# Kernel optimization log

Measured on AMD Instinct MI355X. Metric: run time of the kernel, lower is better.

Reference implementation:

```python
import jax, jax.numpy as jnp
import numpy as np

# graph layout constants
B = 64        # number of graphs
NPG = 512     # nodes per graph
N = B * NPG   # total nodes
DEG = 16      # avg degree
E = N * DEG   # total edges
F_IN = 256
H, C = 4, 64  # heads, per-head dim
K = NPG // 2  # topk pooling keeps ratio=0.5 per graph


def setup_inputs() -> dict:
    key = jax.random.key(0)
    ks = jax.random.split(key, 8)
    x = jax.random.normal(ks[0], (N, F_IN), dtype=jnp.float32)
    # within-graph random edges (src -> dst), contiguous node ids per graph
    offs = jnp.repeat(jnp.arange(B, dtype=jnp.int64) * NPG, NPG * DEG)
    src = offs + jax.random.randint(ks[1], (E,), 0, NPG)
    dst = offs + jax.random.randint(ks[2], (E,), 0, NPG)
    edge_index = jnp.stack([src, dst]).astype(jnp.int64)
    W = jax.random.normal(ks[3], (F_IN, H, C), dtype=jnp.float32) / np.sqrt(F_IN)
    att_src = jax.random.normal(ks[4], (H, C), dtype=jnp.float32) / np.sqrt(C)
    att_dst = jax.random.normal(ks[5], (H, C), dtype=jnp.float32) / np.sqrt(C)
    bias = jnp.zeros((H * C,), dtype=jnp.float32)
    bn_gamma = jnp.ones((H * C,), dtype=jnp.float32)
    bn_beta = jnp.zeros((H * C,), dtype=jnp.float32)
    pool_weight = jax.random.normal(ks[6], (H * C,), dtype=jnp.float32) / np.sqrt(H * C)
    return {"x": x, "edge_index": edge_index, "W": W, "att_src": att_src,
            "att_dst": att_dst, "bias": bias, "bn_gamma": bn_gamma,
            "bn_beta": bn_beta, "pool_weight": pool_weight}


def reference(x, edge_index, W, att_src, att_dst, bias, bn_gamma, bn_beta, pool_weight):
    n = x.shape[0]
    # --- GATConv ---
    h = jnp.einsum('nf,fhc->nhc', x, W)                 # [N,H,C]
    a_src = jnp.sum(h * att_src, axis=-1)               # [N,H]
    a_dst = jnp.sum(h * att_dst, axis=-1)               # [N,H]
    loops = jnp.arange(n, dtype=edge_index.dtype)        # add_self_loops=True default
    src = jnp.concatenate([edge_index[0], loops])
    dst = jnp.concatenate([edge_index[1], loops])
    e = jax.nn.leaky_relu(a_src[src] + a_dst[dst], 0.2)  # [E+N,H]
    # scatter-softmax over edges grouped by destination node
    emax = jax.ops.segment_max(e, dst, num_segments=n)
    ex = jnp.exp(e - emax[dst])
    den = jax.ops.segment_sum(ex, dst, num_segments=n)
    alpha = ex / (den[dst] + 1e-16)                      # [E+N,H]
    msg = alpha[:, :, None] * h[src]                     # [E+N,H,C]
    out = jax.ops.segment_sum(msg, dst, num_segments=n)  # [N,H,C]
    feat = out.reshape(n, H * C) + bias                  # concat heads
    # --- ReLU + BatchNorm (batch stats, training mode) ---
    feat = jax.nn.relu(feat)
    mean = jnp.mean(feat, axis=0)
    var = jnp.var(feat, axis=0)
    feat = (feat - mean) * jax.lax.rsqrt(var + 1e-5) * bn_gamma + bn_beta
    # --- TopKPooling (score = x.w/||w||, keep top ratio per graph, gate by tanh) ---
    score = feat @ pool_weight / jnp.linalg.norm(pool_weight)  # [N]
    top_s, top_i = jax.lax.top_k(score.reshape(B, NPG), K)     # [B,K]
    fg = feat.reshape(B, NPG, H * C)
    sel = jnp.take_along_axis(fg, top_i[:, :, None], axis=1)    # [B,K,HC]
    pooled = sel * jnp.tanh(top_s)[:, :, None]
    return pooled.reshape(B * K, H * C)
```

## Files before the change

### kernel.cpp

```cpp
#include <hip/hip_runtime.h>
#include <math.h>

#define N_NODES 32768
#define NPG 512
#define NGRAPH 64
#define KKEEP 256
#define CAP 64

typedef __attribute__((ext_vector_type(8))) short short8;
typedef __attribute__((ext_vector_type(4))) float f32x4;

__device__ __forceinline__ unsigned short f2bf(float v) {
  unsigned u = __builtin_bit_cast(unsigned, v);
  u = (u + 0x7FFFu + ((u >> 16) & 1u)) >> 16;
  return (unsigned short)u;
}
__device__ __forceinline__ float bf2f(unsigned short u) {
  unsigned v = ((unsigned)u) << 16;
  return __builtin_bit_cast(float, v);
}

__device__ __forceinline__ void async_cp16(unsigned short* l, const unsigned short* g) {
  __builtin_amdgcn_global_load_lds(
      (const __attribute__((address_space(1))) unsigned int*)g,
      (__attribute__((address_space(3))) unsigned int*)l, 16, 0, 0);
}

__device__ __forceinline__ void block_barrier() {
  __builtin_amdgcn_sched_barrier(0);
  asm volatile("s_barrier" ::: "memory");
  __builtin_amdgcn_sched_barrier(0);
}
__device__ __forceinline__ void wait_all() {
  asm volatile("s_waitcnt vmcnt(0) lgkmcnt(0)" ::: "memory");
  __builtin_amdgcn_sched_barrier(0);
}

__global__ __launch_bounds__(256) void k_conv(
    const float* __restrict__ W,
    unsigned short* __restrict__ wth, unsigned short* __restrict__ wtl,
    unsigned short* __restrict__ wtll, int* __restrict__ cnt) {
  const int t = threadIdx.x;
  if (blockIdx.x >= 64) {
    int i = (blockIdx.x - 64) * 1024 + t * 4;
    *(int4*)&cnt[i] = make_int4(0, 0, 0, 0);
    return;
  }
  int n = blockIdx.x * 4 + (t >> 6);
  int k = (t & 63) * 4;
  unsigned short hb[4], lb[4], qb[4];
#pragma unroll
  for (int j = 0; j < 4; j++) {
    float v = W[(size_t)(k + j) * 256 + n];
    unsigned short hh = f2bf(v);
    float e1 = v - bf2f(hh);
    unsigned short ll = f2bf(e1);
    float e2 = e1 - bf2f(ll);
    hb[j] = hh; lb[j] = ll; qb[j] = f2bf(e2);
  }
  *(uint2*)&wth[(size_t)n * 256 + k] = *(uint2*)&hb[0];
  *(uint2*)&wtl[(size_t)n * 256 + k] = *(uint2*)&lb[0];
  *(uint2*)&wtll[(size_t)n * 256 + k] = *(uint2*)&qb[0];
}

#define A_STR 129
#define B_BASE 12384
#define B_SZ 12288
__global__ __launch_bounds__(512, 4) void k_gemm_hist(
    const float* __restrict__ x,
    const unsigned short* __restrict__ wth, const unsigned short* __restrict__ wtl,
    const unsigned short* __restrict__ wtll,
    const float* __restrict__ attS, const float* __restrict__ attD,
    float* __restrict__ h, float* __restrict__ a_src, float* __restrict__ a_dst,
    const int* __restrict__ ei, int E, int* __restrict__ cnt,
    unsigned short* __restrict__ nbr) {
  __shared__ unsigned short lds[36960];
  const int t = threadIdx.x;
  const int bid = blockIdx.x;
  if (bid % 3 != 0) {
    int ord = bid - bid / 3 - 1;
    int e = ord * 512 + t;
    if (e < E) {
      int s = ei[e];
      int d = ei[E + e];
      int slot = atomicAdd(&cnt[d], 1);
      if (slot < CAP) nbr[(size_t)d * CAP + slot] = (unsigned short)(s & (NPG - 1));
    }
    return;
  }
  const int g = bid / 3;
  const int p = (3 * g) & 7;
  const int mb = p * 32 + (g >> 4);
  const int nh = (g >> 3) & 1;
  const int row0 = mb * 128;
  const int wid = t >> 6, lane = t & 63;
  const int q = lane >> 4, ln = lane & 15;
  const int wm = (wid >> 1) * 32, wn = (wid & 1) * 64;
  const int sr = t >> 2, scq = t & 3;
  f32x4 acc[2][4] = {};

  {
    size_t ga = (size_t)(row0 + sr) * 256 + scq * 8;
    float4 f0 = *(const float4*)&x[ga];
    float4 f1 = *(const float4*)&x[ga + 4];
    float ff[8] = {f0.x, f0.y, f0.z, f0.w, f1.x, f1.y, f1.z, f1.w};
    unsigned short hs[8], ls[8], qs[8];
#pragma unroll
    for (int j = 0; j < 8; j++) {
      unsigned short hh = f2bf(ff[j]);
      float e1 = ff[j] - bf2f(hh);
      unsigned short ll = f2bf(e1);
      float e2 = e1 - bf2f(ll);
      hs[j] = hh; ls[j] = ll; qs[j] = f2bf(e2);
    }
    *(uint4*)&lds[((0 * 4 + scq) * A_STR + sr) * 8] = *(uint4*)&hs[0];
    *(uint4*)&lds[((1 * 4 + scq) * A_STR + sr) * 8] = *(uint4*)&ls[0];
    *(uint4*)&lds[((2 * 4 + scq) * A_STR + sr) * 8] = *(uint4*)&qs[0];
    size_t gb = (size_t)(nh * 128 + (t & 127)) * 256 + (t >> 7) * 8;
    async_cp16(&lds[B_BASE + 0 * 4096 + t * 8], &wth[gb]);
    async_cp16(&lds[B_BASE + 1 * 4096 + t * 8], &wtl[gb]);
    async_cp16(&lds[B_BASE + 2 * 4096 + t * 8], &wtll[gb]);
  }
  wait_all();
  block_barrier();

  for (int kc = 0; kc < 8; kc++) {
    const int cur = kc & 1;
    float4 f0, f1;
    if (kc < 7) {
      const int k1 = (kc + 1) * 32;
      size_t ga = (size_t)(row0 + sr) * 256 + k1 + scq * 8;
      f0 = *(const float4*)&x[ga];
      f1 = *(const float4*)&x[ga + 4];
      unsigned short* bb = &lds[B_BASE + (cur ^ 1) * B_SZ];
      size_t gb = (size_t)(nh * 128 + (t & 127)) * 256 + k1 + (t >> 7) * 8;
      async_cp16(&bb[0 * 4096 + t * 8], &wth[gb]);
      async_cp16(&bb[1 * 4096 + t * 8], &wtl[gb]);
      async_cp16(&bb[2 * 4096 + t * 8], &wtll[gb]);
    }
    const unsigned short* bc = &lds[B_BASE + cur * B_SZ];
    short8 ah[2], al[2], aq[2];
#pragma unroll
    for (int mt = 0; mt < 2; mt++) {
      int r = wm + mt * 16 + ln;
      ah[mt] = *(const short8*)&lds[((0 * 4 + q) * A_STR + r) * 8];
      al[mt] = *(const short8*)&lds[((1 * 4 + q) * A_STR + r) * 8];
      aq[mt] = *(const short8*)&lds[((2 * 4 + q) * A_STR + r) * 8];
    }
#pragma unroll
    for (int nt = 0; nt < 4; nt++) {
      int r = wn + nt * 16 + ln;
      short8 bh = *(const short8*)&bc[0 * 4096 + (q * 128 + r) * 8];
      short8 bl = *(const short8*)&bc[1 * 4096 + (q * 128 + r) * 8];
      short8 bq = *(const short8*)&bc[2 * 4096 + (q * 128 + r) * 8];
#pragma unroll
      for (int mt = 0; mt < 2; mt++) {
        acc[mt][nt] = __builtin_amdgcn_mfma_f32_16x16x32_bf16(ah[mt], bh, acc[mt][nt], 0, 0, 0);
        acc[mt][nt] = __builtin_amdgcn_mfma_f32_16x16x32_bf16(ah[mt], bl, acc[mt][nt], 0, 0, 0);
        acc[mt][nt] = __builtin_amdgcn_mfma_f32_16x16x32_bf16(al[mt], bh, acc[mt][nt], 0, 0, 0);
        acc[mt][nt] = __builtin_amdgcn_mfma_f32_16x16x32_bf16(ah[mt], bq, acc[mt][nt], 0, 0, 0);
        acc[mt][nt] = __builtin_amdgcn_mfma_f32_16x16x32_bf16(al[mt], bl, acc[mt][nt], 0, 0, 0);
        acc[mt][nt] = __builtin_amdgcn_mfma_f32_16x16x32_bf16(aq[mt], bh, acc[mt][nt], 0, 0, 0);
      }
    }
    unsigned short hs[8], ls[8], qs[8];
    if (kc < 7) {
      float ff[8] = {f0.x, f0.y, f0.z, f0.w, f1.x, f1.y, f1.z, f1.w};
#pragma unroll
      for (int j = 0; j < 8; j++) {
        unsigned short hh = f2bf(ff[j]);
        float e1 = ff[j] - bf2f(hh);
        unsigned short ll = f2bf(e1);
        float e2 = e1 - bf2f(ll);
        hs[j] = hh; ls[j] = ll; qs[j] = f2bf(e2);
      }
    }
    block_barrier();
    if (kc < 7) {
      *(uint4*)&lds[((0 * 4 + scq) * A_STR + sr) * 8] = *(uint4*)&hs[0];
      *(uint4*)&lds[((1 * 4 + scq) * A_STR + sr) * 8] = *(uint4*)&ls[0];
      *(uint4*)&lds[((2 * 4 + scq) * A_STR + sr) * 8] = *(uint4*)&qs[0];
    }
    wait_all();
    block_barrier();
  }

  const int head = nh * 2 + (wid & 1);
  float sA[4], sD[4];
#pragma unroll
  for (int nt = 0; nt < 4; nt++) {
    int n = nh * 128 + wn + nt * 16 + ln;
    sA[nt] = attS[n];
    sD[nt] = attD[n];
  }
  float2* epi = (float2*)lds;
#pragma unroll
  for (int mt = 0; mt < 2; mt++) {
#pragma unroll
    for (int reg = 0; reg < 4; reg++) {
      int m = row0 + wm + mt * 16 + q * 4 + reg;
      float ps = 0.f, pd = 0.f;
#pragma unroll
      for (int nt = 0; nt < 4; nt++) {
        float v = acc[mt][nt][reg];
        h[(size_t)m * 256 + nh * 128 + wn + nt * 16 + ln] = v;
        ps = fmaf(v, sA[nt], ps);
        pd = fmaf(v, sD[nt], pd);
      }
      epi[(((wid * 4 + q) * 8) + mt * 4 + reg) * 18 + (ln ^ (q * 4))] =
          make_float2(ps, pd);
    }
  }
  __syncthreads();
  if (lane < 32) {
    const int rr2 = lane & 7;
    const int q2 = lane >> 3;
    const int base = (((wid * 4 + q2) * 8) + rr2) * 18;
    float ps = 0.f, pd = 0.f;
#pragma unroll
    for (int i = 0; i < 16; i++) {
      float2 v = epi[base + (i ^ (q2 * 4))];
      ps += v.x;
      pd += v.y;
    }
    int m = row0 + wm + (rr2 >> 2) * 16 + q2 * 4 + (rr2 & 3);
    a_src[m * 4 + head] = ps;
    a_dst[m * 4 + head] = pd;
  }
}

__global__ __launch_bounds__(256) void k_agg(
    const float* __restrict__ h, const float* __restrict__ a_src,
    const float* __restrict__ a_dst, const int* __restrict__ cnt,
    const unsigned short* __restrict__ nbr, const float* __restrict__ bias,
    float* __restrict__ feat) {
  __shared__ float p_lds[4][68][4];
  __shared__ int s_lds[4][68];
  const int wv = threadIdx.x >> 6;
  const int lane = threadIdx.x & 63;
  int nb = (blockIdx.x & 7) * (N_NODES / 4 / 8) + (blockIdx.x >> 3);
  const int node = nb * 4 + wv;
  const int head = lane >> 4;
  const int li = lane & 15;
  const int c0 = lane * 4;
  const int base = node & ~(NPG - 1);
  const float ad = a_dst[node * 4 + head];
  int n = cnt[node];
  if (n > CAP) n = CAP;
  float e_reg[5];
  int srcs[5];
  int nit = 0;
  float m = -1e30f;
  for (int j = li; j <= n; j += 16) {
    int s = (j < n) ? base + (int)nbr[(size_t)node * CAP + j] : node;
    float e = a_src[s * 4 + head] + ad;
    e = (e > 0.f) ? e : 0.2f * e;
    srcs[nit] = s;
    e_reg[nit++] = e;
    m = fmaxf(m, e);
  }
#pragma unroll
  for (int d = 1; d < 16; d <<= 1) m = fmaxf(m, __shfl_xor(m, d, 16));
  float l = 0.f;
  for (int i = 0; i < nit; i++) {
    int j = li + i * 16;
    float p = __expf(e_reg[i] - m);
    l += p;
    p_lds[wv][j][head] = p;
    if (head == 0) s_lds[wv][j] = srcs[i];
  }
#pragma unroll
  for (int d = 1; d < 16; d <<= 1) l += __shfl_xor(l, d, 16);
  const float linv = 1.f / (l + 1e-16f);
  __builtin_amdgcn_s_waitcnt(0);
  float4 acc0 = make_float4(0.f, 0.f, 0.f, 0.f);
  float4 acc1 = make_float4(0.f, 0.f, 0.f, 0.f);
  int j = 0;
  for (; j + 1 <= n; j += 2) {
    float p0 = p_lds[wv][j][head];
    float p1 = p_lds[wv][j + 1][head];
    int s0 = s_lds[wv][j];
    int s1 = s_lds[wv][j + 1];
    float4 h0 = *(const float4*)&h[(size_t)s0 * 256 + c0];
    float4 h1 = *(const float4*)&h[(size_t)s1 * 256 + c0];
    acc0.x = fmaf(p0, h0.x, acc0.x); acc1.x = fmaf(p1, h1.x, acc1.x);
    acc0.y = fmaf(p0, h0.y, acc0.y); acc1.y = fmaf(p1, h1.y, acc1.y);
    acc0.z = fmaf(p0, h0.z, acc0.z); acc1.z = fmaf(p1, h1.z, acc1.z);
    acc0.w = fmaf(p0, h0.w, acc0.w); acc1.w = fmaf(p1, h1.w, acc1.w);
  }
  if (j <= n) {
    float p0 = p_lds[wv][j][head];
    int s0 = s_lds[wv][j];
    float4 h0 = *(const float4*)&h[(size_t)s0 * 256 + c0];
    acc0.x = fmaf(p0, h0.x, acc0.x);
    acc0.y = fmaf(p0, h0.y, acc0.y);
    acc0.z = fmaf(p0, h0.z, acc0.z);
    acc0.w = fmaf(p0, h0.w, acc0.w);
  }
  const float4 b4 = *(const float4*)&bias[c0];
  float4 o;
  o.x = fmaxf(fmaf(acc0.x + acc1.x, linv, b4.x), 0.f);
  o.y = fmaxf(fmaf(acc0.y + acc1.y, linv, b4.y), 0.f);
  o.z = fmaxf(fmaf(acc0.z + acc1.z, linv, b4.z), 0.f);
  o.w = fmaxf(fmaf(acc0.w + acc1.w, linv, b4.w), 0.f);
  *(float4*)&feat[(size_t)node * 256 + c0] = o;
}

__global__ __launch_bounds__(64) void k_bn_partial(const float* __restrict__ feat,
                                                   double* __restrict__ psum,
                                                   double* __restrict__ psq) {
  const int chunk = blockIdx.x >> 2;
  const int c = (blockIdx.x & 3) * 64 + threadIdx.x;
  const int r0 = chunk * 128;
  double s = 0.0, q = 0.0;
  for (int i = 0; i < 128; i++) {
    double v = (double)feat[(size_t)(r0 + i) * 256 + c];
    s += v;
    q += v * v;
  }
  psum[chunk * 256 + c] = s;
  psq[chunk * 256 + c] = q;
}

__global__ __launch_bounds__(1024) void k_bn_final(
    const double* __restrict__ psum, const double* __restrict__ psq,
    const float* __restrict__ gam, const float* __restrict__ bet,
    const float* __restrict__ pw, float* __restrict__ cA, float* __restrict__ cB,
    float* __restrict__ sv) {
  __shared__ double reds[4][256];
  __shared__ double redq[4][256];
  __shared__ double wsq[256];
  __shared__ double sb[256];
  const int t = threadIdx.x;
  const int c = t & 255, sl = t >> 8;
  double s = 0.0, q = 0.0;
  for (int i = sl * 64; i < sl * 64 + 64; i++) {
    s += psum[i * 256 + c];
    q += psq[i * 256 + c];
  }
  reds[sl][c] = s;
  redq[sl][c] = q;
  if (sl == 0) {
    double w = (double)pw[c];
    wsq[c] = w * w;
  }
  __syncthreads();
  if (t == 0) {
    double nn = 0.0;
    for (int i = 0; i < 256; i++) nn += wsq[i];
    wsq[0] = sqrt(nn);
  }
  __syncthreads();
  if (sl == 0) {
    s = reds[0][c] + reds[1][c] + reds[2][c] + reds[3][c];
    q = redq[0][c] + redq[1][c] + redq[2][c] + redq[3][c];
    double mean = s / (double)N_NODES;
    double var = q / (double)N_NODES - mean * mean;
    double a = (double)gam[c] / sqrt(var + 1e-5);
    double cb = (double)bet[c] - mean * a;
    cA[c] = (float)a;
    cB[c] = (float)cb;
    double pwnv = (double)pw[c] / wsq[0];
    sv[c] = (float)(a * pwnv);
    sb[c] = cb * pwnv;
  }
  __syncthreads();
  if (t == 0) {
    double s0 = 0.0;
    for (int i = 0; i < 256; i++) s0 += sb[i];
    sv[256] = (float)s0;
  }
}

__global__ __launch_bounds__(256) void k_score(
    const float* __restrict__ feat, const float* __restrict__ sv,
    float* __restrict__ score) {
  const int lane = threadIdx.x & 63;
  const int node = blockIdx.x * 4 + (threadIdx.x >> 6);
  const int c0 = lane * 4;
  float4 f = *(const float4*)&feat[(size_t)node * 256 + c0];
  float4 w = *(const float4*)&sv[c0];
  float p = f.x * w.x + f.y * w.y + f.z * w.z + f.w * w.w;
#pragma unroll
  for (int d = 1; d < 64; d <<= 1) p += __shfl_xor(p, d, 64);
  if (lane == 0) score[node] = p + sv[256];
}

__global__ __launch_bounds__(256) void k_topk(
    const float* __restrict__ score, const float* __restrict__ feat,
    const float* __restrict__ cA, const float* __restrict__ cB,
    float* __restrict__ out) {
  __shared__ float ss[NPG];
  __shared__ int rnk[64];
  __shared__ float gt[64];
  const int g = blockIdx.x >> 3;
  const int part = blockIdx.x & 7;
  const int t = threadIdx.x;
  ss[t] = score[g * NPG + t];
  ss[t + 256] = score[g * NPG + t + 256];
  __syncthreads();
  const int ln = t & 3;
  const int ndl = part * 64 + (t >> 2);
  const float s = ss[ndl];
  int rank = 0;
  for (int j = ln * 128; j < ln * 128 + 128; j++) {
    float sj = ss[j];
    rank += (sj > s || (sj == s && j < ndl)) ? 1 : 0;
  }
  rank += __shfl_xor(rank, 1);
  rank += __shfl_xor(rank, 2);
  if (ln == 0) {
    rnk[t >> 2] = rank;
    gt[t >> 2] = tanhf(s);
  }
  __syncthreads();
  for (int idx = t; idx < 64 * 64; idx += 256) {
    int r = idx >> 6;
    int rank2 = rnk[r];
    if (rank2 < KKEEP) {
      int c4 = (idx & 63) * 4;
      int node = g * NPG + part * 64 + r;
      float4 f = *(const float4*)&feat[(size_t)node * 256 + c4];
      float4 a = *(const float4*)&cA[c4];
      float4 b = *(const float4*)&cB[c4];
      float tg = gt[r];
      float4 o;
      o.x = fmaf(f.x, a.x, b.x) * tg;
      o.y = fmaf(f.y, a.y, b.y) * tg;
      o.z = fmaf(f.z, a.z, b.z) * tg;
      o.w = fmaf(f.w, a.w, b.w) * tg;
      *(float4*)&out[(size_t)(g * KKEEP + rank2) * 256 + c4] = o;
    }
  }
}

extern "C" void kernel_launch(void* const* d_in, const int* in_sizes, int n_in,
                              void* d_out, int out_size, void* d_ws, size_t ws_size,
                              hipStream_t stream) {
  const float* x    = (const float*)d_in[0];
  const int*   ei   = (const int*)d_in[1];
  const float* W    = (const float*)d_in[2];
  const float* attS = (const float*)d_in[3];
  const float* attD = (const float*)d_in[4];
  const float* bias = (const float*)d_in[5];
  const float* gam  = (const float*)d_in[6];
  const float* bet  = (const float*)d_in[7];
  const float* pw   = (const float*)d_in[8];
  float* out = (float*)d_out;
  const int E = in_sizes[1] / 2;

  char* p = (char*)d_ws;
  float* h     = (float*)p; p += (size_t)N_NODES * 256 * 4;
  float* feat  = (float*)p; p += (size_t)N_NODES * 256 * 4;
  float* a_src = (float*)p; p += (size_t)N_NODES * 4 * 4;
  float* a_dst = (float*)p; p += (size_t)N_NODES * 4 * 4;
  float* score = (float*)p; p += (size_t)N_NODES * 4;
  double* psum = (double*)p; p += (size_t)256 * 256 * 8;
  double* psq  = (double*)p; p += (size_t)256 * 256 * 8;
  float* cA    = (float*)p; p += 256 * 4;
  float* cB    = (float*)p; p += 256 * 4;
  float* sv    = (float*)p; p += 260 * 4;
  unsigned short* wth  = (unsigned short*)p; p += (size_t)256 * 256 * 2;
  unsigned short* wtl  = (unsigned short*)p; p += (size_t)256 * 256 * 2;
  unsigned short* wtll = (unsigned short*)p; p += (size_t)256 * 256 * 2;
  int* cnt     = (int*)p;   p += (size_t)N_NODES * 4;
  unsigned short* nbr = (unsigned short*)p; p += (size_t)N_NODES * CAP * 2;

  k_conv<<<96, 256, 0, stream>>>(W, wth, wtl, wtll, cnt);
  k_gemm_hist<<<1536, 512, 0, stream>>>(x, wth, wtl, wtll, attS, attD,
                                        h, a_src, a_dst, ei, E, cnt, nbr);
  k_agg<<<N_NODES / 4, 256, 0, stream>>>(h, a_src, a_dst, cnt, nbr, bias, feat);
  k_bn_partial<<<1024, 64, 0, stream>>>(feat, psum, psq);
  k_bn_final<<<1, 1024, 0, stream>>>(psum, psq, gam, bet, pw, cA, cB, sv);
  k_score<<<N_NODES / 4, 256, 0, stream>>>(feat, sv, score);
  k_topk<<<NGRAPH * 8, 256, 0, stream>>>(score, feat, cA, cB, out);
}
```

Baseline: 213.4 us.

## Halve GEMM block threads with 64x64 per-wave tiles and split histogram blocks

The fused GEMM/histogram kernel now runs 256-thread blocks instead of 512. Each GEMM wave computes a 64x64 output tile (4x4 MFMA fragments) instead of 32x64, so each thread loads and converts two A rows per K step. The edge-histogram blocks are moved to a contiguous range after the 512 GEMM blocks instead of being interleaved with them. The aim is more MFMA work per LDS fragment load and fewer threads per block, at the cost of higher register pressure (acc doubles) and less interleaving of the memory-bound histogram with the GEMM work.

```diff
diff --git a/kernel.cpp b/kernel.cpp
--- a/kernel.cpp
+++ b/kernel.cpp
@@ -66,7 +66,7 @@
 #define A_STR 129
 #define B_BASE 12384
 #define B_SZ 12288
-__global__ __launch_bounds__(512, 4) void k_gemm_hist(
+__global__ __launch_bounds__(256, 2) void k_gemm_hist(
     const float* __restrict__ x,
     const unsigned short* __restrict__ wth, const unsigned short* __restrict__ wtl,
     const unsigned short* __restrict__ wtll,
@@ -77,9 +77,8 @@
   __shared__ unsigned short lds[36960];
   const int t = threadIdx.x;
   const int bid = blockIdx.x;
-  if (bid % 3 != 0) {
-    int ord = bid - bid / 3 - 1;
-    int e = ord * 512 + t;
+  if (bid >= 512) {
+    int e = (bid - 512) * 256 + t;
     if (e < E) {
       int s = ei[e];
       int d = ei[E + e];
@@ -88,19 +87,19 @@
     }
     return;
   }
-  const int g = bid / 3;
-  const int p = (3 * g) & 7;
-  const int mb = p * 32 + (g >> 4);
-  const int nh = (g >> 3) & 1;
+  const int mb = (bid & 7) * 32 + (bid >> 4);
+  const int nh = (bid >> 3) & 1;
   const int row0 = mb * 128;
   const int wid = t >> 6, lane = t & 63;
   const int q = lane >> 4, ln = lane & 15;
-  const int wm = (wid >> 1) * 32, wn = (wid & 1) * 64;
-  const int sr = t >> 2, scq = t & 3;
-  f32x4 acc[2][4] = {};
-
-  {
-    size_t ga = (size_t)(row0 + sr) * 256 + scq * 8;
+  const int wm = (wid >> 1) * 64, wn = (wid & 1) * 64;
+  f32x4 acc[4][4] = {};
+
+#pragma unroll
+  for (int i = 0; i < 2; i++) {
+    int c = i * 256 + t;
+    int r = c >> 2, cq = c & 3;
+    size_t ga = (size_t)(row0 + r) * 256 + cq * 8;
     float4 f0 = *(const float4*)&x[ga];
     float4 f1 = *(const float4*)&x[ga + 4];
     float ff[8] = {f0.x, f0.y, f0.z, f0.w, f1.x, f1.y, f1.z, f1.w};
@@ -113,35 +112,40 @@
       float e2 = e1 - bf2f(ll);
       hs[j] = hh; ls[j] = ll; qs[j] = f2bf(e2);
     }
-    *(uint4*)&lds[((0 * 4 + scq) * A_STR + sr) * 8] = *(uint4*)&hs[0];
-    *(uint4*)&lds[((1 * 4 + scq) * A_STR + sr) * 8] = *(uint4*)&ls[0];
-    *(uint4*)&lds[((2 * 4 + scq) * A_STR + sr) * 8] = *(uint4*)&qs[0];
-    size_t gb = (size_t)(nh * 128 + (t & 127)) * 256 + (t >> 7) * 8;
-    async_cp16(&lds[B_BASE + 0 * 4096 + t * 8], &wth[gb]);
-    async_cp16(&lds[B_BASE + 1 * 4096 + t * 8], &wtl[gb]);
-    async_cp16(&lds[B_BASE + 2 * 4096 + t * 8], &wtll[gb]);
+    *(uint4*)&lds[((0 * 4 + cq) * A_STR + r) * 8] = *(uint4*)&hs[0];
+    *(uint4*)&lds[((1 * 4 + cq) * A_STR + r) * 8] = *(uint4*)&ls[0];
+    *(uint4*)&lds[((2 * 4 + cq) * A_STR + r) * 8] = *(uint4*)&qs[0];
+    size_t gb = (size_t)(nh * 128 + (c & 127)) * 256 + (c >> 7) * 8;
+    async_cp16(&lds[B_BASE + 0 * 4096 + c * 8], &wth[gb]);
+    async_cp16(&lds[B_BASE + 1 * 4096 + c * 8], &wtl[gb]);
+    async_cp16(&lds[B_BASE + 2 * 4096 + c * 8], &wtll[gb]);
   }
   wait_all();
   block_barrier();
 
   for (int kc = 0; kc < 8; kc++) {
     const int cur = kc & 1;
-    float4 f0, f1;
+    float4 nf[4];
     if (kc < 7) {
       const int k1 = (kc + 1) * 32;
-      size_t ga = (size_t)(row0 + sr) * 256 + k1 + scq * 8;
-      f0 = *(const float4*)&x[ga];
-      f1 = *(const float4*)&x[ga + 4];
       unsigned short* bb = &lds[B_BASE + (cur ^ 1) * B_SZ];
-      size_t gb = (size_t)(nh * 128 + (t & 127)) * 256 + k1 + (t >> 7) * 8;
-      async_cp16(&bb[0 * 4096 + t * 8], &wth[gb]);
-      async_cp16(&bb[1 * 4096 + t * 8], &wtl[gb]);
-      async_cp16(&bb[2 * 4096 + t * 8], &wtll[gb]);
+#pragma unroll
+      for (int i = 0; i < 2; i++) {
+        int c = i * 256 + t;
+        int r = c >> 2, cq = c & 3;
+        size_t ga = (size_t)(row0 + r) * 256 + k1 + cq * 8;
+        nf[i * 2 + 0] = *(const float4*)&x[ga];
+        nf[i * 2 + 1] = *(const float4*)&x[ga + 4];
+        size_t gb = (size_t)(nh * 128 + (c & 127)) * 256 + k1 + (c >> 7) * 8;
+        async_cp16(&bb[0 * 4096 + c * 8], &wth[gb]);
+        async_cp16(&bb[1 * 4096 + c * 8], &wtl[gb]);
+        async_cp16(&bb[2 * 4096 + c * 8], &wtll[gb]);
+      }
     }
     const unsigned short* bc = &lds[B_BASE + cur * B_SZ];
-    short8 ah[2], al[2], aq[2];
-#pragma unroll
-    for (int mt = 0; mt < 2; mt++) {
+    short8 ah[4], al[4], aq[4];
+#pragma unroll
+    for (int mt = 0; mt < 4; mt++) {
       int r = wm + mt * 16 + ln;
       ah[mt] = *(const short8*)&lds[((0 * 4 + q) * A_STR + r) * 8];
       al[mt] = *(const short8*)&lds[((1 * 4 + q) * A_STR + r) * 8];
@@ -154,7 +158,7 @@
       short8 bl = *(const short8*)&bc[1 * 4096 + (q * 128 + r) * 8];
       short8 bq = *(const short8*)&bc[2 * 4096 + (q * 128 + r) * 8];
 #pragma unroll
-      for (int mt = 0; mt < 2; mt++) {
+      for (int mt = 0; mt < 4; mt++) {
         acc[mt][nt] = __builtin_amdgcn_mfma_f32_16x16x32_bf16(ah[mt], bh, acc[mt][nt], 0, 0, 0);
         acc[mt][nt] = __builtin_amdgcn_mfma_f32_16x16x32_bf16(ah[mt], bl, acc[mt][nt], 0, 0, 0);
         acc[mt][nt] = __builtin_amdgcn_mfma_f32_16x16x32_bf16(al[mt], bh, acc[mt][nt], 0, 0, 0);
@@ -163,23 +167,32 @@
         acc[mt][nt] = __builtin_amdgcn_mfma_f32_16x16x32_bf16(aq[mt], bh, acc[mt][nt], 0, 0, 0);
       }
     }
-    unsigned short hs[8], ls[8], qs[8];
+    unsigned short hs[2][8], ls[2][8], qs[2][8];
     if (kc < 7) {
-      float ff[8] = {f0.x, f0.y, f0.z, f0.w, f1.x, f1.y, f1.z, f1.w};
-#pragma unroll
-      for (int j = 0; j < 8; j++) {
-        unsigned short hh = f2bf(ff[j]);
-        float e1 = ff[j] - bf2f(hh);
-        unsigned short ll = f2bf(e1);
-        float e2 = e1 - bf2f(ll);
-        hs[j] = hh; ls[j] = ll; qs[j] = f2bf(e2);
+#pragma unroll
+      for (int i = 0; i < 2; i++) {
+        float ff[8] = {nf[i * 2].x, nf[i * 2].y, nf[i * 2].z, nf[i * 2].w,
+                       nf[i * 2 + 1].x, nf[i * 2 + 1].y, nf[i * 2 + 1].z, nf[i * 2 + 1].w};
+#pragma unroll
+        for (int j = 0; j < 8; j++) {
+          unsigned short hh = f2bf(ff[j]);
+          float e1 = ff[j] - bf2f(hh);
+          unsigned short ll = f2bf(e1);
+          float e2 = e1 - bf2f(ll);
+          hs[i][j] = hh; ls[i][j] = ll; qs[i][j] = f2bf(e2);
+        }
       }
     }
     block_barrier();
     if (kc < 7) {
-      *(uint4*)&lds[((0 * 4 + scq) * A_STR + sr) * 8] = *(uint4*)&hs[0];
-      *(uint4*)&lds[((1 * 4 + scq) * A_STR + sr) * 8] = *(uint4*)&ls[0];
-      *(uint4*)&lds[((2 * 4 + scq) * A_STR + sr) * 8] = *(uint4*)&qs[0];
+#pragma unroll
+      for (int i = 0; i < 2; i++) {
+        int c = i * 256 + t;
+        int r = c >> 2, cq = c & 3;
+        *(uint4*)&lds[((0 * 4 + cq) * A_STR + r) * 8] = *(uint4*)&hs[i][0];
+        *(uint4*)&lds[((1 * 4 + cq) * A_STR + r) * 8] = *(uint4*)&ls[i][0];
+        *(uint4*)&lds[((2 * 4 + cq) * A_STR + r) * 8] = *(uint4*)&qs[i][0];
+      }
     }
     wait_all();
     block_barrier();
@@ -195,7 +208,7 @@
   }
   float2* epi = (float2*)lds;
 #pragma unroll
-  for (int mt = 0; mt < 2; mt++) {
+  for (int mt = 0; mt < 4; mt++) {
 #pragma unroll
     for (int reg = 0; reg < 4; reg++) {
       int m = row0 + wm + mt * 16 + q * 4 + reg;
@@ -207,15 +220,14 @@
         ps = fmaf(v, sA[nt], ps);
         pd = fmaf(v, sD[nt], pd);
       }
-      epi[(((wid * 4 + q) * 8) + mt * 4 + reg) * 18 + (ln ^ (q * 4))] =
+      epi[(((wid * 4 + q) * 16) + mt * 4 + reg) * 18 + (ln ^ (q * 4))] =
           make_float2(ps, pd);
     }
   }
   __syncthreads();
-  if (lane < 32) {
-    const int rr2 = lane & 7;
-    const int q2 = lane >> 3;
-    const int base = (((wid * 4 + q2) * 8) + rr2) * 18;
+  {
+    const int q2 = lane >> 4, rr = lane & 15;
+    const int base = (((wid * 4 + q2) * 16) + rr) * 18;
     float ps = 0.f, pd = 0.f;
 #pragma unroll
     for (int i = 0; i < 16; i++) {
@@ -223,7 +235,7 @@
       ps += v.x;
       pd += v.y;
     }
-    int m = row0 + wm + (rr2 >> 2) * 16 + q2 * 4 + (rr2 & 3);
+    int m = row0 + wm + (rr >> 2) * 16 + q2 * 4 + (rr & 3);
     a_src[m * 4 + head] = ps;
     a_dst[m * 4 + head] = pd;
   }
@@ -467,7 +479,7 @@
   unsigned short* nbr = (unsigned short*)p; p += (size_t)N_NODES * CAP * 2;
 
   k_conv<<<96, 256, 0, stream>>>(W, wth, wtl, wtll, cnt);
-  k_gemm_hist<<<1536, 512, 0, stream>>>(x, wth, wtl, wtll, attS, attD,
+  k_gemm_hist<<<2560, 256, 0, stream>>>(x, wth, wtl, wtll, attS, attD,
                                         h, a_src, a_dst, ei, E, cnt, nbr);
   k_agg<<<N_NODES / 4, 256, 0, stream>>>(h, a_src, a_dst, cnt, nbr, bias, feat);
   k_bn_partial<<<1024, 64, 0, stream>>>(feat, psum, psq);
```

New measurement: 206.0 us. 3.4% less time.
